# Kernel optimization log

Measured on AMD Instinct MI355X. Metric: run time of the kernel, lower is better.

## Reference

```python
import jax, jax.numpy as jnp
import numpy as np

K = 256
TAU = 1.0


def setup_inputs() -> dict:
    key = jax.random.key(0)
    scores = jax.random.normal(key, (32, 2048), dtype=jnp.float32)
    return {"scores": scores}


def reference(scores) -> jnp.ndarray:
    # scores: [B, dim]
    bsize, dim = scores.shape
    s = scores[:, :, None]  # [B, dim, 1]
    # B_i = sum_j |s_i - s_j|  -> [B, dim, 1]
    A = jnp.abs(s - scores[:, None, :])  # [B, dim, dim]
    Bsum = jnp.sum(A, axis=-1, keepdims=True)  # [B, dim, 1]
    # scaling: (dim + 1 - 2*(i+1)) for i in 0..k-1
    scaling = (dim + 1 - 2 * (jnp.arange(K) + 1)).astype(scores.dtype)  # [k]
    C = s * scaling[None, None, :]  # [B, dim, k] (outer product)
    P_max = jnp.transpose(C - Bsum, (0, 2, 1))  # [B, k, dim]
    P_hat = jax.nn.softmax(P_max / TAU, axis=-1)
    return P_hat
```

## Files before the change

### kernel.cpp

```cpp
#include <hip/hip_runtime.h>
#include <math.h>

#define DIM 2048
#define NB 32
#define NK 256

typedef float vf4 __attribute__((ext_vector_type(4)));

__global__ __launch_bounds__(256) void bsum_kernel(const float* __restrict__ scores,
                                                   float* __restrict__ bsum) {
    const int b = blockIdx.y;
    const int i = blockIdx.x * 256 + threadIdx.x;
    const float* __restrict__ row = scores + b * DIM;
    const float xi = row[i];

    float a0 = 0.f, a1 = 0.f, a2 = 0.f, a3 = 0.f;
    #pragma unroll 8
    for (int j = 0; j < DIM; j += 4) {
        a0 += fabsf(xi - row[j + 0]);
        a1 += fabsf(xi - row[j + 1]);
        a2 += fabsf(xi - row[j + 2]);
        a3 += fabsf(xi - row[j + 3]);
    }
    bsum[b * DIM + i] = (a0 + a1) + (a2 + a3);
}

__global__ __launch_bounds__(256) void softmax_kernel(const float* __restrict__ scores,
                                                      const float* __restrict__ bsum,
                                                      float* __restrict__ out) {
    const int b = blockIdx.y;
    const int w = threadIdx.x >> 6;
    const int t = threadIdx.x & 63;
    const int k = blockIdx.x * 4 + w;
    const float scale = (float)(DIM - 1 - 2 * k);

    const vf4* __restrict__ s4  = (const vf4*)(scores + b * DIM);
    const vf4* __restrict__ bs4 = (const vf4*)(bsum   + b * DIM);

    float e[32];
    #pragma unroll
    for (int q = 0; q < 8; ++q) {
        const vf4 sv = s4[t + 64 * q];
        const vf4 bv = bs4[t + 64 * q];
        e[4 * q + 0] = fmaf(sv.x, scale, -bv.x);
        e[4 * q + 1] = fmaf(sv.y, scale, -bv.y);
        e[4 * q + 2] = fmaf(sv.z, scale, -bv.z);
        e[4 * q + 3] = fmaf(sv.w, scale, -bv.w);
    }

    float m0 = e[0], m1 = e[1], m2 = e[2], m3 = e[3];
    #pragma unroll
    for (int j = 4; j < 32; j += 4) {
        m0 = fmaxf(m0, e[j + 0]);
        m1 = fmaxf(m1, e[j + 1]);
        m2 = fmaxf(m2, e[j + 2]);
        m3 = fmaxf(m3, e[j + 3]);
    }
    float m = fmaxf(fmaxf(m0, m1), fmaxf(m2, m3));
    #pragma unroll
    for (int off = 32; off > 0; off >>= 1) m = fmaxf(m, __shfl_xor(m, off, 64));

    float s0 = 0.f, s1 = 0.f, s2 = 0.f, s3 = 0.f;
    #pragma unroll
    for (int j = 0; j < 32; j += 4) {
        e[j + 0] = __expf(e[j + 0] - m); s0 += e[j + 0];
        e[j + 1] = __expf(e[j + 1] - m); s1 += e[j + 1];
        e[j + 2] = __expf(e[j + 2] - m); s2 += e[j + 2];
        e[j + 3] = __expf(e[j + 3] - m); s3 += e[j + 3];
    }
    float s = (s0 + s1) + (s2 + s3);
    #pragma unroll
    for (int off = 32; off > 0; off >>= 1) s += __shfl_xor(s, off, 64);

    const float inv = 1.f / s;
    vf4* o4 = (vf4*)(out + ((size_t)(b * NK + k)) * DIM);
    #pragma unroll
    for (int q = 0; q < 8; ++q) {
        vf4 o;
        o.x = e[4 * q + 0] * inv;
        o.y = e[4 * q + 1] * inv;
        o.z = e[4 * q + 2] * inv;
        o.w = e[4 * q + 3] * inv;
        __builtin_nontemporal_store(o, &o4[t + 64 * q]);
    }
}

extern "C" void kernel_launch(void* const* d_in, const int* in_sizes, int n_in,
                              void* d_out, int out_size, void* d_ws, size_t ws_size,
                              hipStream_t stream) {
    const float* scores = (const float*)d_in[0];
    float* out  = (float*)d_out;
    float* bsum = (float*)d_ws;

    bsum_kernel<<<dim3(8, NB), 256, 0, stream>>>(scores, bsum);
    softmax_kernel<<<dim3(NK / 4, NB), 256, 0, stream>>>(scores, bsum, out);
}
```

Baseline: 107.7 us.

## Split pairwise abs-sum over j-chunks with LDS tiling and atomic accumulation

Bsum kernel is restructured: each thread handles 4 i-values, j is split into 4 chunks of 512 staged in LDS, and partial sums are combined via atomicAdd into a memset-zeroed buffer. This raises register reuse (4x4 outer product per LDS load) and keeps the grid at 256 blocks over the i and j split. It adds a memset launch and atomics, and makes the summation order nondeterministic. The softmax output store also switches from nontemporal to a regular store.

Result: faster. 91.86 us (-14.7%).

```diff
diff --git a/kernel.cpp b/kernel.cpp
--- a/kernel.cpp
+++ b/kernel.cpp
@@ -9,20 +9,30 @@
 
 __global__ __launch_bounds__(256) void bsum_kernel(const float* __restrict__ scores,
                                                    float* __restrict__ bsum) {
-    const int b = blockIdx.y;
-    const int i = blockIdx.x * 256 + threadIdx.x;
+    __shared__ vf4 srow[128];
+    const int b  = blockIdx.z;
+    const int j0 = blockIdx.y * 512;
+    const int i0 = blockIdx.x * 1024;
     const float* __restrict__ row = scores + b * DIM;
-    const float xi = row[i];
 
+    if (threadIdx.x < 128) srow[threadIdx.x] = ((const vf4*)(row + j0))[threadIdx.x];
+    __syncthreads();
+
+    const vf4 xi = ((const vf4*)(row + i0))[threadIdx.x];
     float a0 = 0.f, a1 = 0.f, a2 = 0.f, a3 = 0.f;
-    #pragma unroll 8
-    for (int j = 0; j < DIM; j += 4) {
-        a0 += fabsf(xi - row[j + 0]);
-        a1 += fabsf(xi - row[j + 1]);
-        a2 += fabsf(xi - row[j + 2]);
-        a3 += fabsf(xi - row[j + 3]);
+    #pragma unroll 4
+    for (int jj = 0; jj < 128; ++jj) {
+        const vf4 xj = srow[jj];
+        a0 += (fabsf(xi.x - xj.x) + fabsf(xi.x - xj.y)) + (fabsf(xi.x - xj.z) + fabsf(xi.x - xj.w));
+        a1 += (fabsf(xi.y - xj.x) + fabsf(xi.y - xj.y)) + (fabsf(xi.y - xj.z) + fabsf(xi.y - xj.w));
+        a2 += (fabsf(xi.z - xj.x) + fabsf(xi.z - xj.y)) + (fabsf(xi.z - xj.z) + fabsf(xi.z - xj.w));
+        a3 += (fabsf(xi.w - xj.x) + fabsf(xi.w - xj.y)) + (fabsf(xi.w - xj.z) + fabsf(xi.w - xj.w));
     }
-    bsum[b * DIM + i] = (a0 + a1) + (a2 + a3);
+    float* dst = bsum + b * DIM + i0 + threadIdx.x * 4;
+    atomicAdd(dst + 0, a0);
+    atomicAdd(dst + 1, a1);
+    atomicAdd(dst + 2, a2);
+    atomicAdd(dst + 3, a3);
 }
 
 __global__ __launch_bounds__(256) void softmax_kernel(const float* __restrict__ scores,
@@ -81,7 +91,7 @@
         o.y = e[4 * q + 1] * inv;
         o.z = e[4 * q + 2] * inv;
         o.w = e[4 * q + 3] * inv;
-        __builtin_nontemporal_store(o, &o4[t + 64 * q]);
+        o4[t + 64 * q] = o;
     }
 }
 
@@ -92,6 +102,7 @@
     float* out  = (float*)d_out;
     float* bsum = (float*)d_ws;
 
-    bsum_kernel<<<dim3(8, NB), 256, 0, stream>>>(scores, bsum);
+    hipMemsetAsync(bsum, 0, (size_t)NB * DIM * sizeof(float), stream);
+    bsum_kernel<<<dim3(2, 4, NB), 256, 0, stream>>>(scores, bsum);
     softmax_kernel<<<dim3(NK / 4, NB), 256, 0, stream>>>(scores, bsum, out);
 }
```
